# Kernel optimization log

Hardware: AMD Instinct MI355X
Metric: run time of the kernel (lower is better)

The kernel has to match this reference:

```python
import jax, jax.numpy as jnp
import numpy as np

# static config
B, T, D, E, K = 2, 2048, 1024, 8, 2
CAPACITY_FACTOR = 1.25
NT = B * T  # num_tokens
_cap = K * NT / E * CAPACITY_FACTOR
_cap += _cap % 2
EXP_CAP = int(_cap)  # 1280


def setup_inputs() -> dict:
    key = jax.random.key(0)
    k1, k2 = jax.random.split(key)
    x = jax.random.normal(k1, (B, T, D), dtype=jnp.float32)
    w_router = jax.random.normal(k2, (E, D), dtype=jnp.float32) * 0.02
    return {"x": x, "w_router": w_router}


def reference(x, w_router):
    # router logits: (B,T,E)
    logits = jnp.einsum('btd,ed->bte', x, w_router)

    # top-k selection
    topk_logits, topk_idx = jax.lax.top_k(logits, K)  # (B,T,K)

    # softmax over only the top-k logits (others masked to -inf), matching
    # torch's full_like(-inf).scatter_(topk) then softmax
    in_topk = jax.nn.one_hot(topk_idx, E, dtype=logits.dtype).sum(axis=-2) > 0  # (B,T,E)
    masked = jnp.where(in_topk, logits, -jnp.inf)
    router_probs = jax.nn.softmax(masked, axis=-1)  # (B,T,E)

    # expert assignment mask: (K, NT, E)
    exp_mask = jax.nn.one_hot(topk_idx, E, dtype=jnp.int32)  # (B,T,K,E)
    exp_mask = exp_mask.reshape(NT, K, E).transpose(1, 0, 2)

    # rank of each token within its expert's buffer (priority: k=0 tokens first)
    rank = jnp.cumsum(exp_mask.reshape(K * NT, E), axis=0) - 1
    rank = rank.reshape(K, NT, E)

    # drop tokens that exceed expert capacity
    exp_mask = exp_mask * (rank < EXP_CAP).astype(jnp.int32)
    used_cap = jnp.sum(exp_mask, axis=(0, 1))  # (E,)

    # per-(k, token) slot index within the assigned expert's buffer
    slot = jnp.sum(exp_mask * rank, axis=-1)  # (K, NT) int

    probs_flat = router_probs.reshape(NT, E)
    exp_weights = exp_mask.astype(probs_flat.dtype) * probs_flat[None]  # (K,NT,E)

    # cb_weight[t, e, c] = sum_k exp_weights[k,t,e] * (slot[k,t] == c)
    # scatter-add instead of materializing the one-hot (K,NT,EXP_CAP) tensor
    t_idx = jnp.broadcast_to(jnp.arange(NT)[None, :], (K, NT))
    cb_weight = jnp.zeros((NT, E, EXP_CAP), dtype=probs_flat.dtype)
    cb_weight = cb_weight.at[t_idx, :, slot].add(exp_weights)  # (NT,E,EXP_CAP)

    sec_mask = cb_weight != 0  # bool dispatch mask
    return used_cap, cb_weight, sec_mask
```

## Files before the change

### kernel.cpp

```cpp
#include <hip/hip_runtime.h>
#include <hip/hip_bf16.h>
#include <math.h>

#define NT      4096
#define DD      1024
#define EE      8
#define KK      2
#define CAP     1280
#define CBN     (NT * EE * CAP)

#define K2T     1024
#define JPT     (KK * NT / K2T)

__device__ __forceinline__ int swz(int j) { return j ^ ((j >> 5) & 31); }

__global__ __launch_bounds__(256) void logits_kernel(
    const float* __restrict__ x,
    const float* __restrict__ w,
    int* __restrict__ e0, int* __restrict__ e1,
    float* __restrict__ p0, float* __restrict__ p1)
{
    __shared__ float wl[EE * DD];

    for (int i = threadIdx.x; i < EE * DD / 4; i += 256)
        reinterpret_cast<float4*>(wl)[i] = reinterpret_cast<const float4*>(w)[i];
    __syncthreads();

    const int wave = threadIdx.x >> 6;
    const int lane = threadIdx.x & 63;
    const int wid  = blockIdx.x * 4 + wave;

    for (int t = wid; t < NT; t += gridDim.x * 4) {
        const float4* xt = reinterpret_cast<const float4*>(x + (size_t)t * DD);
        float acc[EE];
        #pragma unroll
        for (int e = 0; e < EE; ++e) acc[e] = 0.0f;

        #pragma unroll
        for (int ii = 0; ii < DD / 4 / 64; ++ii) {
            const int i = ii * 64 + lane;
            const float4 xv = xt[i];
            #pragma unroll
            for (int e = 0; e < EE; ++e) {
                const float4 wv = reinterpret_cast<const float4*>(wl + e * DD)[i];
                acc[e] += xv.x * wv.x + xv.y * wv.y + xv.z * wv.z + xv.w * wv.w;
            }
        }

        #pragma unroll
        for (int e = 0; e < EE; ++e) {
            float v = acc[e];
            #pragma unroll
            for (int off = 32; off > 0; off >>= 1) v += __shfl_xor(v, off);
            acc[e] = v;
        }

        if (lane == 0) {
            int b0 = 0; float l0 = acc[0];
            #pragma unroll
            for (int e = 1; e < EE; ++e) { if (acc[e] > l0) { l0 = acc[e]; b0 = e; } }
            int b1 = -1; float l1 = -INFINITY;
            #pragma unroll
            for (int e = 0; e < EE; ++e) { if (e != b0 && acc[e] > l1) { l1 = acc[e]; b1 = e; } }

            const float z  = expf(l1 - l0);
            const float pa = 1.0f / (1.0f + z);
            const float pb = z * pa;

            e0[t] = b0; e1[t] = b1;
            p0[t] = pa; p1[t] = pb;
        }
    }
}

__global__ __launch_bounds__(K2T) void rank_scatter_kernel(
    const int* __restrict__ e0, const int* __restrict__ e1,
    const float* __restrict__ p0, const float* __restrict__ p1,
    float* __restrict__ out)
{
    __shared__ int   se[KK * NT];
    __shared__ float sp[KK * NT];
    __shared__ unsigned long long wsumA[16], wsumB[16];

    const int tid = threadIdx.x;

    #pragma unroll
    for (int k = 0; k < NT / K2T; ++k) {
        const int i = k * K2T + tid;
        se[swz(i)]      = e0[i];
        se[swz(NT + i)] = e1[i];
        sp[swz(i)]      = p0[i];
        sp[swz(NT + i)] = p1[i];
    }
    __syncthreads();

    const int base = tid * JPT;
    unsigned long long ca = 0ull, cb = 0ull;
    #pragma unroll
    for (int i = 0; i < JPT; ++i) {
        const int e = se[swz(base + i)];
        if (e < 4) ca += 1ull << (16 * e);
        else       cb += 1ull << (16 * (e - 4));
    }

    unsigned long long sa = ca, sb = cb;
    #pragma unroll
    for (int off = 1; off < 64; off <<= 1) {
        const unsigned long long ta = __shfl_up(sa, off);
        const unsigned long long tb = __shfl_up(sb, off);
        if ((tid & 63) >= off) { sa += ta; sb += tb; }
    }
    const int wv = tid >> 6;
    if ((tid & 63) == 63) { wsumA[wv] = sa; wsumB[wv] = sb; }
    __syncthreads();

    unsigned long long preA = 0ull, preB = 0ull;
    #pragma unroll
    for (int k = 0; k < 16; ++k) {
        if (k < wv) { preA += wsumA[k]; preB += wsumB[k]; }
    }
    unsigned long long ra = preA + sa - ca;
    unsigned long long rb = preB + sb - cb;

    #pragma unroll
    for (int i = 0; i < JPT; ++i) {
        const int j = base + i;
        const int e = se[swz(j)];
        int rank;
        if (e < 4) { rank = (int)((ra >> (16 * e)) & 0xFFFF);       ra += 1ull << (16 * e); }
        else       { rank = (int)((rb >> (16 * (e - 4))) & 0xFFFF); rb += 1ull << (16 * (e - 4)); }
        if (rank < CAP) {
            const float p = sp[swz(j)];
            if (p != 0.0f) {
                const int t = j & (NT - 1);
                const size_t idx = (size_t)t * (EE * CAP) + (size_t)e * CAP + (size_t)rank;
                out[8 + idx] = p;
                out[8 + (size_t)CBN + idx] = 1.0f;
            }
        }
    }

    if (tid < EE) {
        unsigned long long totA = 0ull, totB = 0ull;
        #pragma unroll
        for (int k = 0; k < 16; ++k) { totA += wsumA[k]; totB += wsumB[k]; }
        const int e = tid;
        const int tot = (e < 4) ? (int)((totA >> (16 * e)) & 0xFFFF)
                                : (int)((totB >> (16 * (e - 4))) & 0xFFFF);
        out[e] = (float)((tot < CAP) ? tot : CAP);
    }
}

extern "C" void kernel_launch(void* const* d_in, const int* in_sizes, int n_in,
                              void* d_out, int out_size, void* d_ws, size_t ws_size,
                              hipStream_t stream) {
    const float* x = (const float*)d_in[0];
    const float* w = (const float*)d_in[1];
    float* out = (float*)d_out;

    char* ws = (char*)d_ws;
    int*   e0 = (int*)(ws);
    int*   e1 = (int*)(ws + 16 * 1024);
    float* p0 = (float*)(ws + 32 * 1024);
    float* p1 = (float*)(ws + 48 * 1024);

    hipMemsetAsync(d_out, 0, (size_t)out_size * sizeof(float), stream);

    logits_kernel<<<512, 256, 0, stream>>>(x, w, e0, e1, p0, p1);

    rank_scatter_kernel<<<1, K2T, 0, stream>>>(e0, e1, p0, p1, out);
}
```

Before: 79.53 us.

## Fuse output zeroing, router logits and rank scatter into one kernel

Replaces the full-output hipMemsetAsync and the two kernels with a single 256-block kernel. Each wave computes one token's router logits and top-2 probabilities, then zeroes its share of the output with nontemporal vector stores. A global atomic counter picks the last block to finish, and that block does the prefix-sum ranking and the scatter, while the memset now only clears the counter. This removes extra launches and lets zeroing overlap with the logits compute. In exchange, it relies on acquire/release ordering for correctness, and the serial rank phase stays on a single block.

```diff
diff --git a/kernel.cpp b/kernel.cpp
--- a/kernel.cpp
+++ b/kernel.cpp
@@ -9,28 +9,43 @@
 #define CAP     1280
 #define CBN     (NT * EE * CAP)
 
-#define K2T     1024
-#define JPT     (KK * NT / K2T)
+#define NB      256
+#define BT      1024
+#define WPB     (BT / 64)
+#define NWAVE   (NB * WPB)
+#define F4TOT   (2 * CBN / 4)
+#define F4PW    (F4TOT / NWAVE)
+#define JPT     (KK * NT / BT)
+
+typedef float vf4 __attribute__((ext_vector_type(4)));
 
 __device__ __forceinline__ int swz(int j) { return j ^ ((j >> 5) & 31); }
 
-__global__ __launch_bounds__(256) void logits_kernel(
+__global__ __launch_bounds__(BT) void fused_all_kernel(
     const float* __restrict__ x,
     const float* __restrict__ w,
+    float* __restrict__ out,
+    unsigned* __restrict__ cnt,
     int* __restrict__ e0, int* __restrict__ e1,
     float* __restrict__ p0, float* __restrict__ p1)
 {
-    __shared__ float wl[EE * DD];
+    __shared__ union {
+        float wl[EE * DD];
+        struct { int se[KK * NT]; float sp[KK * NT]; } s2;
+    } u;
+    __shared__ unsigned long long wsumA[WPB], wsumB[WPB];
+    __shared__ int lastflag;
 
-    for (int i = threadIdx.x; i < EE * DD / 4; i += 256)
-        reinterpret_cast<float4*>(wl)[i] = reinterpret_cast<const float4*>(w)[i];
+    const int tid  = threadIdx.x;
+    const int wave = tid >> 6;
+    const int lane = tid & 63;
+
+    for (int i = tid; i < EE * DD / 4; i += BT)
+        reinterpret_cast<float4*>(u.wl)[i] = reinterpret_cast<const float4*>(w)[i];
     __syncthreads();
 
-    const int wave = threadIdx.x >> 6;
-    const int lane = threadIdx.x & 63;
-    const int wid  = blockIdx.x * 4 + wave;
-
-    for (int t = wid; t < NT; t += gridDim.x * 4) {
+    const int t = blockIdx.x * WPB + wave;
+    {
         const float4* xt = reinterpret_cast<const float4*>(x + (size_t)t * DD);
         float acc[EE];
         #pragma unroll
@@ -42,7 +57,7 @@
             const float4 xv = xt[i];
             #pragma unroll
             for (int e = 0; e < EE; ++e) {
-                const float4 wv = reinterpret_cast<const float4*>(wl + e * DD)[i];
+                const float4 wv = reinterpret_cast<const float4*>(u.wl + e * DD)[i];
                 acc[e] += xv.x * wv.x + xv.y * wv.y + xv.z * wv.z + xv.w * wv.w;
             }
         }
@@ -71,26 +86,32 @@
             p0[t] = pa; p1[t] = pb;
         }
     }
-}
 
-__global__ __launch_bounds__(K2T) void rank_scatter_kernel(
-    const int* __restrict__ e0, const int* __restrict__ e1,
-    const float* __restrict__ p0, const float* __restrict__ p1,
-    float* __restrict__ out)
-{
-    __shared__ int   se[KK * NT];
-    __shared__ float sp[KK * NT];
-    __shared__ unsigned long long wsumA[16], wsumB[16];
+    {
+        const int gw = blockIdx.x * WPB + wave;
+        vf4* dst = reinterpret_cast<vf4*>(out + 8) + (size_t)gw * F4PW + lane;
+        const vf4 zv = {0.0f, 0.0f, 0.0f, 0.0f};
+        #pragma unroll 8
+        for (int it = 0; it < F4PW / 64; ++it)
+            __builtin_nontemporal_store(zv, dst + it * 64);
+    }
 
-    const int tid = threadIdx.x;
+    __syncthreads();
+    if (tid == 0) {
+        const unsigned old = __hip_atomic_fetch_add(cnt, 1u, __ATOMIC_ACQ_REL,
+                                                    __HIP_MEMORY_SCOPE_AGENT);
+        lastflag = (old == NB - 1);
+    }
+    __syncthreads();
+    if (!lastflag) return;
 
     #pragma unroll
-    for (int k = 0; k < NT / K2T; ++k) {
-        const int i = k * K2T + tid;
-        se[swz(i)]      = e0[i];
-        se[swz(NT + i)] = e1[i];
-        sp[swz(i)]      = p0[i];
-        sp[swz(NT + i)] = p1[i];
+    for (int k = 0; k < NT / BT; ++k) {
+        const int i = k * BT + tid;
+        u.s2.se[swz(i)]      = e0[i];
+        u.s2.se[swz(NT + i)] = e1[i];
+        u.s2.sp[swz(i)]      = p0[i];
+        u.s2.sp[swz(NT + i)] = p1[i];
     }
     __syncthreads();
 
@@ -98,7 +119,7 @@
     unsigned long long ca = 0ull, cb = 0ull;
     #pragma unroll
     for (int i = 0; i < JPT; ++i) {
-        const int e = se[swz(base + i)];
+        const int e = u.s2.se[swz(base + i)];
         if (e < 4) ca += 1ull << (16 * e);
         else       cb += 1ull << (16 * (e - 4));
     }
@@ -110,14 +131,13 @@
         const unsigned long long tb = __shfl_up(sb, off);
         if ((tid & 63) >= off) { sa += ta; sb += tb; }
     }
-    const int wv = tid >> 6;
-    if ((tid & 63) == 63) { wsumA[wv] = sa; wsumB[wv] = sb; }
+    if ((tid & 63) == 63) { wsumA[wave] = sa; wsumB[wave] = sb; }
     __syncthreads();
 
     unsigned long long preA = 0ull, preB = 0ull;
     #pragma unroll
-    for (int k = 0; k < 16; ++k) {
-        if (k < wv) { preA += wsumA[k]; preB += wsumB[k]; }
+    for (int k = 0; k < WPB; ++k) {
+        if (k < wave) { preA += wsumA[k]; preB += wsumB[k]; }
     }
     unsigned long long ra = preA + sa - ca;
     unsigned long long rb = preB + sb - cb;
@@ -125,15 +145,15 @@
     #pragma unroll
     for (int i = 0; i < JPT; ++i) {
         const int j = base + i;
-        const int e = se[swz(j)];
+        const int e = u.s2.se[swz(j)];
         int rank;
         if (e < 4) { rank = (int)((ra >> (16 * e)) & 0xFFFF);       ra += 1ull << (16 * e); }
         else       { rank = (int)((rb >> (16 * (e - 4))) & 0xFFFF); rb += 1ull << (16 * (e - 4)); }
         if (rank < CAP) {
-            const float p = sp[swz(j)];
+            const float p = u.s2.sp[swz(j)];
             if (p != 0.0f) {
-                const int t = j & (NT - 1);
-                const size_t idx = (size_t)t * (EE * CAP) + (size_t)e * CAP + (size_t)rank;
+                const int tt = j & (NT - 1);
+                const size_t idx = (size_t)tt * (EE * CAP) + (size_t)e * CAP + (size_t)rank;
                 out[8 + idx] = p;
                 out[8 + (size_t)CBN + idx] = 1.0f;
             }
@@ -143,7 +163,7 @@
     if (tid < EE) {
         unsigned long long totA = 0ull, totB = 0ull;
         #pragma unroll
-        for (int k = 0; k < 16; ++k) { totA += wsumA[k]; totB += wsumB[k]; }
+        for (int k = 0; k < WPB; ++k) { totA += wsumA[k]; totB += wsumB[k]; }
         const int e = tid;
         const int tot = (e < 4) ? (int)((totA >> (16 * e)) & 0xFFFF)
                                 : (int)((totB >> (16 * (e - 4))) & 0xFFFF);
@@ -159,14 +179,13 @@
     float* out = (float*)d_out;
 
     char* ws = (char*)d_ws;
-    int*   e0 = (int*)(ws);
-    int*   e1 = (int*)(ws + 16 * 1024);
-    float* p0 = (float*)(ws + 32 * 1024);
-    float* p1 = (float*)(ws + 48 * 1024);
+    unsigned* cnt = (unsigned*)(ws);
+    int*   e0 = (int*)(ws + 1 * 1024);
+    int*   e1 = (int*)(ws + 17 * 1024);
+    float* p0 = (float*)(ws + 33 * 1024);
+    float* p1 = (float*)(ws + 49 * 1024);
 
-    hipMemsetAsync(d_out, 0, (size_t)out_size * sizeof(float), stream);
+    hipMemsetAsync(cnt, 0, 64, stream);
 
-    logits_kernel<<<512, 256, 0, stream>>>(x, w, e0, e1, p0, p1);
-
-    rank_scatter_kernel<<<1, K2T, 0, stream>>>(e0, e1, p0, p1, out);
+    fused_all_kernel<<<NB, BT, 0, stream>>>(x, w, out, cnt, e0, e1, p0, p1);
 }
```

Result: slower. 114.9 us (+44.5%).
